# Performance work log

Measured on AMD Instinct MI355X. Metric: run time of the kernel, lower is better.

The kernel has to match this reference:

```python
import jax, jax.numpy as jnp
import numpy as np

B, T, NC, NK, H, W = 2, 4, 3, 16, 180, 320
K = 3
PAD = 1
SCALE = 4
K2 = K * K
CIN_D = T * NK  # deformable conv input channels = group_of_frames * num_kernels


def conv2d(x, w, b=None, pad=PAD):
    y = jax.lax.conv_general_dilated(
        x, w, (1, 1), [(pad, pad), (pad, pad)],
        dimension_numbers=('NCHW', 'OIHW', 'NCHW'))
    if b is not None:
        y = y + b[None, :, None, None]
    return y


def convlstm(X, w, b, W_ci, W_cf, W_co):
    # X: (B, T, NC, H, W) -> (B, T, NK, H, W); peephole ConvLSTM
    Bn = X.shape[0]
    h0 = jnp.zeros((Bn, NK, H, W), X.dtype)
    c0 = jnp.zeros_like(h0)

    def step(carry, xt):
        h, c = carry
        g = conv2d(jnp.concatenate([xt, h], axis=1), w, b)  # (B, 4*NK, H, W)
        ig, fg, cg, og = jnp.split(g, 4, axis=1)
        i = jax.nn.sigmoid(ig + W_ci * c)
        f = jax.nn.sigmoid(fg + W_cf * c)
        c = f * c + i * jnp.tanh(cg)
        o = jax.nn.sigmoid(og + W_co * c)
        h = o * jnp.tanh(c)
        return (h, c), h

    _, hs = jax.lax.scan(step, (h0, c0), jnp.swapaxes(X, 0, 1))
    return jnp.swapaxes(hs, 0, 1)  # (B, T, NK, H, W)


def deform_conv(x, off_w, off_b, mod_w, mod_b, w, b):
    # Modulated deformable conv v2 (torchvision deform_conv2d semantics)
    Bn, Cin, Hi, Wi = x.shape
    off = conv2d(x, off_w, off_b).reshape(Bn, K2, 2, Hi, Wi)  # (dy, dx) per tap
    mask = 2.0 * jax.nn.sigmoid(conv2d(x, mod_w, mod_b))       # (B, K2, H, W)
    dy, dx = off[:, :, 0], off[:, :, 1]
    ky, kx = jnp.meshgrid(jnp.arange(K), jnp.arange(K), indexing='ij')
    base_y = jnp.arange(Hi, dtype=x.dtype)[None, None, :, None] - PAD + ky.reshape(1, K2, 1, 1).astype(x.dtype)
    base_x = jnp.arange(Wi, dtype=x.dtype)[None, None, None, :] - PAD + kx.reshape(1, K2, 1, 1).astype(x.dtype)
    py = base_y + dy  # (B, K2, H, W) float sampling positions
    px = base_x + dx
    y0 = jnp.floor(py)
    x0 = jnp.floor(px)

    def gather(yi, xi):
        valid = ((yi >= 0) & (yi < Hi) & (xi >= 0) & (xi < Wi)).astype(x.dtype)
        yc = jnp.clip(yi, 0, Hi - 1).astype(jnp.int32)
        xc = jnp.clip(xi, 0, Wi - 1).astype(jnp.int32)
        v = jax.vmap(lambda xb, yb, xib: xb[:, yb, xib])(x, yc, xc)  # (B, C, K2, H, W)
        return v * valid[:, None]

    wy1 = py - y0
    wx1 = px - x0
    samp = (((1 - wy1) * (1 - wx1))[:, None] * gather(y0, x0)
            + ((1 - wy1) * wx1)[:, None] * gather(y0, x0 + 1)
            + (wy1 * (1 - wx1))[:, None] * gather(y0 + 1, x0)
            + (wy1 * wx1)[:, None] * gather(y0 + 1, x0 + 1))
    samp = samp * mask[:, None]  # (B, Cin, K2, H, W)
    out = jnp.einsum('bckhw,ock->bohw', samp, w.reshape(w.shape[0], Cin, K2))
    return out + b[None, :, None, None]


def pixel_shuffle(x, r):
    Bn, Crr, Hi, Wi = x.shape
    C = Crr // (r * r)
    x = x.reshape(Bn, C, r, r, Hi, Wi).transpose(0, 1, 4, 2, 5, 3)
    return x.reshape(Bn, C, Hi * r, Wi * r)


def setup_inputs() -> dict:
    key = jax.random.key(0)
    ks = jax.random.split(key, 16)
    s = lambda k, shape, sc=0.05: jax.random.normal(k, shape, jnp.float32) * sc
    return {
        'X': jax.random.uniform(ks[0], (B, T, NC, H, W), jnp.float32),
        'lstm_w': s(ks[1], (4 * NK, NC + NK, K, K)),
        'lstm_b': s(ks[2], (4 * NK,)),
        'W_ci': s(ks[3], (NK, H, W)),
        'W_cf': s(ks[4], (NK, H, W)),
        'W_co': s(ks[5], (NK, H, W)),
        'off_w': s(ks[6], (2 * K2, CIN_D, K, K), 0.01),
        'off_b': jnp.zeros((2 * K2,), jnp.float32),
        'mod_w': s(ks[7], (K2, CIN_D, K, K), 0.01),
        'mod_b': jnp.zeros((K2,), jnp.float32),
        'def_w': s(ks[8], (NK, CIN_D, K, K)),
        'def_b': s(ks[9], (NK,)),
        'out_w': s(ks[10], (NC * SCALE ** 2, NK, K, K)),
        'out_b': s(ks[11], (NC * SCALE ** 2,)),
    }


def reference(X, lstm_w, lstm_b, W_ci, W_cf, W_co, off_w, off_b, mod_w, mod_b, def_w, def_b, out_w, out_b):
    hs = convlstm(X, lstm_w, lstm_b, W_ci, W_cf, W_co)   # (B, T, NK, H, W)
    x = hs.reshape(hs.shape[0], T * NK, H, W)            # chunk(dim=1)+squeeze+cat(dim=1)
    x = deform_conv(x, off_w, off_b, mod_w, mod_b, def_w, def_b)  # (B, NK, H, W)
    x = conv2d(x, out_w, out_b)                          # (B, NC*scale^2, H, W)
    return jnp.clip(pixel_shuffle(x, SCALE), 0.0, 255.0)
```

## Files before the change

### kernel.cpp

```cpp
#include <hip/hip_runtime.h>
#include <hip/hip_bf16.h>

#define Bn 2
#define Tn 4
#define NCc 3
#define NKc 16
#define Hc 180
#define Wc 320
#define HWc (Hc * Wc)
#define NPIX (Bn * HWc)
#define CIN_LSTM 19
#define GATES 64
#define CIN_D 64
#define TAPS_L (CIN_LSTM * 9)
#define TAPS_D (CIN_D * 9)
#define TAPS_O (NKc * 9)

typedef __hip_bfloat16 bf16;
typedef float f32x4 __attribute__((ext_vector_type(4)));
typedef float f32x2 __attribute__((ext_vector_type(2)));

__device__ __forceinline__ float getv(const float* p, long i) { return p[i]; }
__device__ __forceinline__ float getv(const bf16* p, long i) {
    unsigned int u = ((unsigned int)((const unsigned short*)p)[i]) << 16;
    return __uint_as_float(u);
}
__device__ __forceinline__ void putv(float* p, long i, float v) { p[i] = v; }
__device__ __forceinline__ void putv(bf16* p, long i, float v) { p[i] = __float2bfloat16(v); }
__device__ __forceinline__ float sigm(float x) { return 1.0f / (1.0f + __expf(-x)); }
__device__ __forceinline__ float tanh_(float x) { return 1.0f - 2.0f / (__expf(2.0f * x) + 1.0f); }

__device__ __forceinline__ void load4(const float* row, int x0, float* d) {
    const float4 v = *(const float4*)(row + x0);
    d[0] = v.x; d[1] = v.y; d[2] = v.z; d[3] = v.w;
}
__device__ __forceinline__ void load4(const bf16* row, int x0, float* d) {
    ushort4 u = *(const ushort4*)((const unsigned short*)row + x0);
    d[0] = __uint_as_float(((unsigned int)u.x) << 16);
    d[1] = __uint_as_float(((unsigned int)u.y) << 16);
    d[2] = __uint_as_float(((unsigned int)u.z) << 16);
    d[3] = __uint_as_float(((unsigned int)u.w) << 16);
}

__device__ __forceinline__ int xcd_chunked(int i, int nwg) {
    int q = nwg >> 3, r = nwg & 7;
    int xcd = i & 7, idx = i >> 3;
    return (xcd < r ? xcd * (q + 1) : r * (q + 1) + (xcd - r) * q) + idx;
}

__device__ __forceinline__ void om_wait()
{
    asm volatile("s_waitcnt vmcnt(0)" ::: "memory");
    __builtin_amdgcn_sched_barrier(0);
}

__device__ __forceinline__ void om13_issue(
    const float* a0p, const float* a1p, const float* a2p,
    const float* b0p, const float* b1p, const float* b2p,
    const float* l0p, const float* l1p, const float* l2p,
    const float* r0p, const float* r1p, const float* r2p,
    f32x4& A0, f32x4& A1, f32x4& A2, f32x4& B0, f32x4& B1, f32x4& B2,
    float& l0, float& l1, float& l2, float& r0, float& r1, float& r2)
{
    asm volatile(
        "global_load_dwordx4 %[A0], %[a0], off\n\t"
        "global_load_dwordx4 %[A1], %[a1], off\n\t"
        "global_load_dwordx4 %[A2], %[a2], off\n\t"
        "global_load_dwordx4 %[B0], %[b0], off\n\t"
        "global_load_dwordx4 %[B1], %[b1], off\n\t"
        "global_load_dwordx4 %[B2], %[b2], off\n\t"
        "global_load_dword %[L0], %[l0p], off\n\t"
        "global_load_dword %[L1], %[l1p], off\n\t"
        "global_load_dword %[L2], %[l2p], off\n\t"
        "global_load_dword %[R0], %[r0p], off\n\t"
        "global_load_dword %[R1], %[r1p], off\n\t"
        "global_load_dword %[R2], %[r2p], off\n\t"
        : [A0]"=&v"(A0), [A1]"=&v"(A1), [A2]"=&v"(A2),
          [B0]"=&v"(B0), [B1]"=&v"(B1), [B2]"=&v"(B2),
          [L0]"=&v"(l0), [L1]"=&v"(l1), [L2]"=&v"(l2),
          [R0]"=&v"(r0), [R1]"=&v"(r1), [R2]"=&v"(r2)
        : [a0]"v"(a0p), [a1]"v"(a1p), [a2]"v"(a2p),
          [b0]"v"(b0p), [b1]"v"(b1p), [b2]"v"(b2p),
          [l0p]"v"(l0p), [l1p]"v"(l1p), [l2p]"v"(l2p),
          [r0p]"v"(r0p), [r1p]"v"(r1p), [r2p]"v"(r2p));
}

__device__ __forceinline__ void lstm_issue12(
    const float* p0, const float* p1, const float* p2, const float* p3,
    f32x4& a0, float& l0, float& r0,
    f32x4& a1, float& l1, float& r1,
    f32x4& a2, float& l2, float& r2,
    f32x4& a3, float& l3, float& r3)
{
    asm volatile(
        "global_load_dwordx4 %[A0], %[P0], off\n\t"
        "global_load_dword   %[L0], %[P0], off offset:-4\n\t"
        "global_load_dword   %[R0], %[P0], off offset:16\n\t"
        "global_load_dwordx4 %[A1], %[P1], off\n\t"
        "global_load_dword   %[L1], %[P1], off offset:-4\n\t"
        "global_load_dword   %[R1], %[P1], off offset:16\n\t"
        "global_load_dwordx4 %[A2], %[P2], off\n\t"
        "global_load_dword   %[L2], %[P2], off offset:-4\n\t"
        "global_load_dword   %[R2], %[P2], off offset:16\n\t"
        "global_load_dwordx4 %[A3], %[P3], off\n\t"
        "global_load_dword   %[L3], %[P3], off offset:-4\n\t"
        "global_load_dword   %[R3], %[P3], off offset:16\n\t"
        : [A0]"=&v"(a0), [L0]"=&v"(l0), [R0]"=&v"(r0),
          [A1]"=&v"(a1), [L1]"=&v"(l1), [R1]"=&v"(r1),
          [A2]"=&v"(a2), [L2]"=&v"(l2), [R2]"=&v"(r2),
          [A3]"=&v"(a3), [L3]"=&v"(l3), [R3]"=&v"(r3)
        : [P0]"v"(p0), [P1]"v"(p1), [P2]"v"(p2), [P3]"v"(p3));
}

__device__ __forceinline__ void dfm_issue9w(
    const float* base, const int (&o)[9], f32x2 (&v)[9])
{
    asm volatile(
        "global_load_dwordx2 %[V0], %[O0], %[B]\n\t"
        "global_load_dwordx2 %[V1], %[O1], %[B]\n\t"
        "global_load_dwordx2 %[V2], %[O2], %[B]\n\t"
        "global_load_dwordx2 %[V3], %[O3], %[B]\n\t"
        "global_load_dwordx2 %[V4], %[O4], %[B]\n\t"
        "global_load_dwordx2 %[V5], %[O5], %[B]\n\t"
        "global_load_dwordx2 %[V6], %[O6], %[B]\n\t"
        "global_load_dwordx2 %[V7], %[O7], %[B]\n\t"
        "global_load_dwordx2 %[V8], %[O8], %[B]\n\t"
        : [V0]"=&v"(v[0]), [V1]"=&v"(v[1]), [V2]"=&v"(v[2]),
          [V3]"=&v"(v[3]), [V4]"=&v"(v[4]), [V5]"=&v"(v[5]),
          [V6]"=&v"(v[6]), [V7]"=&v"(v[7]), [V8]"=&v"(v[8])
        : [B]"s"(base),
          [O0]"v"(o[0]), [O1]"v"(o[1]), [O2]"v"(o[2]),
          [O3]"v"(o[3]), [O4]"v"(o[4]), [O5]"v"(o[5]),
          [O6]"v"(o[6]), [O7]"v"(o[7]), [O8]"v"(o[8]));
}

__global__ void __launch_bounds__(256) k_detect(const void* lstm_w_raw, int* flag)
{
    __shared__ int bad;
    if (threadIdx.x == 0) bad = 0;
    __syncthreads();
    const unsigned short* u = (const unsigned short*)lstm_w_raw;
    int local = 0;
    for (int i = threadIdx.x; i < GATES * TAPS_L; i += 256) {
        unsigned int f32 = ((unsigned int)u[i]) << 16;
        float v = __uint_as_float(f32);
        if (!(fabsf(v) <= 64.0f)) local = 1;
    }
    if (local) atomicOr(&bad, 1);
    __syncthreads();
    if (threadIdx.x == 0) flag[0] = bad ? 0 : 1;
}

template <typename S>
__device__ __forceinline__ void conv_plane2r(
    const S* __restrict__ src, int cin, int y0, int x0, int kc,
    const float* __restrict__ sw, float (&acc)[2][4][4])
{
    float xs[4][6];
#pragma unroll
    for (int r = 0; r < 4; r++) {
        int yy = y0 - 1 + r;
        if (yy >= 0 && yy < Hc) {
            const S* row = src + (long)yy * Wc;
            xs[r][0] = (x0 > 0) ? getv(row, x0 - 1) : 0.0f;
            load4(row, x0, &xs[r][1]);
            xs[r][5] = (x0 + 4 < Wc) ? getv(row, x0 + 4) : 0.0f;
        } else {
#pragma unroll
            for (int j = 0; j < 6; j++) xs[r][j] = 0.0f;
        }
    }
    float4 wq[9];
#pragma unroll
    for (int t9 = 0; t9 < 9; t9++)
        wq[t9] = *(const float4*)&sw[(((cin * 9 + t9) * 16) + kc) * 4];
#pragma unroll
    for (int ky = 0; ky < 3; ky++) {
#pragma unroll
        for (int kx = 0; kx < 3; kx++) {
            const float4 w = wq[ky * 3 + kx];
#pragma unroll
            for (int px = 0; px < 4; px++) {
                float v0 = xs[ky][px + kx];
                float v1 = xs[ky + 1][px + kx];
                acc[0][0][px] += w.x * v0;  acc[1][0][px] += w.x * v1;
                acc[0][1][px] += w.y * v0;  acc[1][1][px] += w.y * v1;
                acc[0][2][px] += w.z * v0;  acc[1][2][px] += w.z * v1;
                acc[0][3][px] += w.w * v0;  acc[1][3][px] += w.w * v1;
            }
        }
    }
}

template <typename T>
__device__ __forceinline__ void lstm2r_body(
    const T* __restrict__ X, const T* __restrict__ lstm_w, const T* __restrict__ lstm_b,
    const T* __restrict__ Wci, const T* __restrict__ Wcf, const T* __restrict__ Wco,
    float* __restrict__ c_buf, float* __restrict__ xcat, int t,
    float* sw, float* sb)
{
    for (int i = threadIdx.x; i < GATES * TAPS_L; i += 256) {
        int co = i / TAPS_L, tap = i - co * TAPS_L;
        int kc = co & 15, g = co >> 4;
        sw[(tap * 16 + kc) * 4 + g] = getv(lstm_w, i);
    }
    if (threadIdx.x < GATES) sb[threadIdx.x] = getv(lstm_b, threadIdx.x);
    __syncthreads();

    int blk = xcd_chunked(blockIdx.x, Bn * 90 * 5);
    int seg = blk % 5; int rem = blk / 5;
    int yp = rem % 90; int b = rem / 90;
    int y0 = yp * 2;
    int kc = threadIdx.x >> 4, pl = threadIdx.x & 15;
    int x0 = seg * 64 + pl * 4;

    float acc[2][4][4];
#pragma unroll
    for (int px = 0; px < 4; px++) {
#pragma unroll
        for (int r = 0; r < 2; r++) {
            acc[r][0][px] = sb[kc];
            acc[r][1][px] = sb[16 + kc];
            acc[r][2][px] = sb[32 + kc];
            acc[r][3][px] = sb[48 + kc];
        }
    }

    const T* xt = X + (long)(b * Tn + t) * NCc * HWc;
#pragma unroll 1
    for (int cin = 0; cin < NCc; cin++)
        conv_plane2r(xt + (long)cin * HWc, cin, y0, x0, kc, sw, acc);

    if (t > 0) {
        const float* hp = xcat + ((long)b * CIN_D + (t - 1) * NKc) * HWc;
        long ro[4]; float vm[4];
#pragma unroll
        for (int r = 0; r < 4; r++) {
            int yy = y0 - 1 + r;
            vm[r] = (yy >= 0 && yy < Hc) ? 1.0f : 0.0f;
            ro[r] = (long)min(max(yy, 0), Hc - 1) * Wc + x0;
        }
        const float m0 = (x0 > 0) ? 1.0f : 0.0f;
        const float m1 = (x0 + 4 < Wc) ? 1.0f : 0.0f;

#pragma unroll 1
        for (int cin = 0; cin < NKc; cin++) {
            const float* xc = hp + (long)cin * HWc;
            f32x4 a0, a1, a2, a3;
            float l0, l1, l2, l3, rh0, rh1, rh2, rh3;
            lstm_issue12(xc + ro[0], xc + ro[1], xc + ro[2], xc + ro[3],
                         a0, l0, rh0, a1, l1, rh1, a2, l2, rh2, a3, l3, rh3);
            float4 wq[9];
#pragma unroll
            for (int t9 = 0; t9 < 9; t9++)
                wq[t9] = *(const float4*)&sw[((((cin + NCc) * 9 + t9) * 16) + kc) * 4];
            om_wait();
            float xs[4][6];
#pragma unroll
            for (int r = 0; r < 4; r++) {
                const f32x4 a = (r == 0) ? a0 : (r == 1) ? a1 : (r == 2) ? a2 : a3;
                const float ll = (r == 0) ? l0 : (r == 1) ? l1 : (r == 2) ? l2 : l3;
                const float rr = (r == 0) ? rh0 : (r == 1) ? rh1 : (r == 2) ? rh2 : rh3;
                xs[r][0] = ll * vm[r] * m0;
                xs[r][1] = a.x * vm[r]; xs[r][2] = a.y * vm[r];
                xs[r][3] = a.z * vm[r]; xs[r][4] = a.w * vm[r];
                xs[r][5] = rr * vm[r] * m1;
            }
#pragma unroll
            for (int ky = 0; ky < 3; ky++) {
#pragma unroll
                for (int kx = 0; kx < 3; kx++) {
                    const float4 w = wq[ky * 3 + kx];
#pragma unroll
                    for (int px = 0; px < 4; px++) {
                        float v0 = xs[ky][px + kx];
                        float v1 = xs[ky + 1][px + kx];
                        acc[0][0][px] += w.x * v0;  acc[1][0][px] += w.x * v1;
                        acc[0][1][px] += w.y * v0;  acc[1][1][px] += w.y * v1;
                        acc[0][2][px] += w.z * v0;  acc[1][2][px] += w.z * v1;
                        acc[0][3][px] += w.w * v0;  acc[1][3][px] += w.w * v1;
                    }
                }
            }
        }
    }

#pragma unroll
    for (int r = 0; r < 2; r++) {
        int y = y0 + r;
        long pbase = (long)y * Wc + x0;
        float* cb = c_buf + (long)(b * NKc + kc) * HWc + pbase;
        float cprev[4];
        if (t > 0) {
            const float4 cv = *(const float4*)cb;
            cprev[0] = cv.x; cprev[1] = cv.y; cprev[2] = cv.z; cprev[3] = cv.w;
        } else {
            cprev[0] = cprev[1] = cprev[2] = cprev[3] = 0.0f;
        }
        float wci[4], wcf[4], wco[4];
        load4(Wci + (long)kc * HWc + pbase, 0, wci);
        load4(Wcf + (long)kc * HWc + pbase, 0, wcf);
        load4(Wco + (long)kc * HWc + pbase, 0, wco);

        float cn4[4], h4[4];
#pragma unroll
        for (int px = 0; px < 4; px++) {
            float ii = sigm(acc[r][0][px] + wci[px] * cprev[px]);
            float ff = sigm(acc[r][1][px] + wcf[px] * cprev[px]);
            float cn = ff * cprev[px] + ii * tanh_(acc[r][2][px]);
            float oo = sigm(acc[r][3][px] + wco[px] * cn);
            cn4[px] = cn; h4[px] = oo * tanh_(cn);
        }
        *(float4*)cb = make_float4(cn4[0], cn4[1], cn4[2], cn4[3]);
        *(float4*)(xcat + ((long)b * CIN_D + t * NKc + kc) * HWc + pbase) =
            make_float4(h4[0], h4[1], h4[2], h4[3]);
    }
}

__global__ void __launch_bounds__(256) k_lstm2(
    const void* X, const void* lstm_w, const void* lstm_b,
    const void* Wci, const void* Wcf, const void* Wco,
    const int* __restrict__ flag,
    float* c_buf, float* xcat, int t)
{
    __shared__ float sw[TAPS_L * GATES];
    __shared__ float sb[GATES];
    if (flag[0])
        lstm2r_body<bf16>((const bf16*)X, (const bf16*)lstm_w, (const bf16*)lstm_b,
                          (const bf16*)Wci, (const bf16*)Wcf, (const bf16*)Wco,
                          c_buf, xcat, t, sw, sb);
    else
        lstm2r_body<float>((const float*)X, (const float*)lstm_w, (const float*)lstm_b,
                           (const float*)Wci, (const float*)Wcf, (const float*)Wco,
                           c_buf, xcat, t, sw, sb);
}

template <typename T>
__device__ __forceinline__ void offmod13_body(
    const float* __restrict__ xcat,
    const T* __restrict__ off_w, const T* __restrict__ off_b,
    const T* __restrict__ mod_w, const T* __restrict__ mod_b,
    float* __restrict__ offbuf, float* __restrict__ maskbuf,
    float* sw, float* sb)
{
    int rb = xcd_chunked(blockIdx.x, 450);
    int type = rb & 1;
    int chunk = rb >> 1;
    const int nslot = type ? 12 : 16;

    for (int i = threadIdx.x; i < TAPS_D * nslot; i += 256) {
        int tap = i / nslot, j = i - tap * nslot;
        int o = type ? 16 + j : j;
        float v = 0.0f;
        if (o < 18) v = getv(off_w, (long)o * TAPS_D + tap);
        else if (o < 27) v = getv(mod_w, (long)(o - 18) * TAPS_D + tap);
        sw[tap * nslot + j] = v;
    }
    if (threadIdx.x < nslot) {
        int o = (type ? 16 : 0) + threadIdx.x;
        sb[threadIdx.x] = (o < 18) ? getv(off_b, o)
                        : (o < 27 ? getv(mod_b, o - 18) : 0.0f);
    }
    __syncthreads();

    int og = threadIdx.x >> 6, lane = threadIdx.x & 63;

    long pg[2]; pg[0] = (long)chunk * 512 + 4 * lane; pg[1] = pg[0] + 256;
    int bg[2], ppg[2];
    int yo[2][3]; float vm[2][3], mL[2], mR[2];
    const float* xbg[2];
#pragma unroll
    for (int g = 0; g < 2; g++) {
        int b = (int)(pg[g] / HWc);
        int pp = (int)(pg[g] - (long)b * HWc);
        int y = pp / Wc, x = pp - (pp / Wc) * Wc;
        bg[g] = b; ppg[g] = pp;
        xbg[g] = xcat + (long)b * CIN_D * HWc;
#pragma unroll
        for (int ky = 0; ky < 3; ky++) {
            int yy = y + ky - 1;
            vm[g][ky] = (yy >= 0 && yy < Hc) ? 1.0f : 0.0f;
            yo[g][ky] = min(max(yy, 0), Hc - 1) * Wc + x;
        }
        mL[g] = (x > 0) ? 1.0f : 0.0f;
        mR[g] = (x + 4 < Wc) ? 1.0f : 0.0f;
    }
    const float *eLp[3], *eRp[3];
    {
        long pL = (long)chunk * 512;
        int b = (int)(pL / HWc); int pp = (int)(pL - (long)b * HWc);
        int y = pp / Wc, x = pp - (pp / Wc) * Wc;
#pragma unroll
        for (int ky = 0; ky < 3; ky++)
            eLp[ky] = xcat + (long)b * CIN_D * HWc
                    + (long)min(max(y + ky - 1, 0), Hc - 1) * Wc + x - 1;
        long pR = (long)chunk * 512 + 511;
        b = (int)(pR / HWc); pp = (int)(pR - (long)b * HWc);
        y = pp / Wc; x = pp - (pp / Wc) * Wc;
#pragma unroll
        for (int ky = 0; ky < 3; ky++)
            eRp[ky] = xcat + (long)b * CIN_D * HWc
                    + (long)min(max(y + ky - 1, 0), Hc - 1) * Wc + x + 1;
    }

    const int per = type ? 3 : 4;
    int jbase = og * per;
    const int upl = (lane + 63) & 63, dnl = (lane + 1) & 63;

    float acc[4][2][4];
#pragma unroll
    for (int j = 0; j < 4; j++) {
        float bv = (j < per) ? sb[jbase + j] : 0.0f;
#pragma unroll
        for (int g = 0; g < 2; g++)
#pragma unroll
            for (int px = 0; px < 4; px++) acc[j][g][px] = bv;
    }

#pragma unroll 1
    for (int cin = 0; cin < CIN_D; cin++) {
        const long coff = (long)cin * HWc;
        const float* c0 = xbg[0] + coff;
        const float* c1 = xbg[1] + coff;
        f32x4 A[3], B[3]; float el[3], er[3];
        om13_issue(c0 + yo[0][0], c0 + yo[0][1], c0 + yo[0][2],
                   c1 + yo[1][0], c1 + yo[1][1], c1 + yo[1][2],
                   eLp[0] + coff, eLp[1] + coff, eLp[2] + coff,
                   eRp[0] + coff, eRp[1] + coff, eRp[2] + coff,
                   A[0], A[1], A[2], B[0], B[1], B[2],
                   el[0], el[1], el[2], er[0], er[1], er[2]);
        float4 wr4[9]; float3 wr3[9];
        if (type == 0) {
#pragma unroll
            for (int t9 = 0; t9 < 9; t9++)
                wr4[t9] = *(const float4*)&sw[(cin * 9 + t9) * 16 + jbase];
        } else {
#pragma unroll
            for (int t9 = 0; t9 < 9; t9++) {
                const float* wp = &sw[(cin * 9 + t9) * 12 + jbase];
                wr3[t9] = make_float3(wp[0], wp[1], wp[2]);
            }
        }
        om_wait();

        float xs0[3][6], xs1[3][6];
#pragma unroll
        for (int ky = 0; ky < 3; ky++) {
            float aw = A[ky].w, ax = A[ky].x, bw = B[ky].w, bx = B[ky].x;
            float sAw = __shfl(aw, upl);
            float sAx = __shfl(ax, dnl);
            float sBw = __shfl(bw, upl);
            float sBx = __shfl(bx, dnl);
            float B0x = __shfl(bx, 0);
            float A63w = __shfl(aw, 63);
            float g0l = (lane == 0) ? el[ky] : sAw;
            float g0r = (lane == 63) ? B0x : sAx;
            float g1l = (lane == 0) ? A63w : sBw;
            float g1r = (lane == 63) ? er[ky] : sBx;
            float v0 = vm[0][ky], v1 = vm[1][ky];
            xs0[ky][0] = g0l * v0 * mL[0];
            xs0[ky][1] = A[ky].x * v0; xs0[ky][2] = A[ky].y * v0;
            xs0[ky][3] = A[ky].z * v0; xs0[ky][4] = A[ky].w * v0;
            xs0[ky][5] = g0r * v0 * mR[0];
            xs1[ky][0] = g1l * v1 * mL[1];
            xs1[ky][1] = B[ky].x * v1; xs1[ky][2] = B[ky].y * v1;
            xs1[ky][3] = B[ky].z * v1; xs1[ky][4] = B[ky].w * v1;
            xs1[ky][5] = g1r * v1 * mR[1];
        }

        if (type == 0) {
#pragma unroll
            for (int ky = 0; ky < 3; ky++) {
#pragma unroll
                for (int kx = 0; kx < 3; kx++) {
                    const float4 wq = wr4[ky * 3 + kx];
#pragma unroll
                    for (int px = 0; px < 4; px++) {
                        float u = xs0[ky][px + kx];
                        acc[0][0][px] += wq.x * u;
                        acc[1][0][px] += wq.y * u;
                        acc[2][0][px] += wq.z * u;
                        acc[3][0][px] += wq.w * u;
                        float w2 = xs1[ky][px + kx];
                        acc[0][1][px] += wq.x * w2;
                        acc[1][1][px] += wq.y * w2;
                        acc[2][1][px] += wq.z * w2;
                        acc[3][1][px] += wq.w * w2;
                    }
                }
            }
        } else {
#pragma unroll
            for (int ky = 0; ky < 3; ky++) {
#pragma unroll
                for (int kx = 0; kx < 3; kx++) {
                    const float3 wq = wr3[ky * 3 + kx];
#pragma unroll
                    for (int px = 0; px < 4; px++) {
                        float u = xs0[ky][px + kx];
                        acc[0][0][px] += wq.x * u;
                        acc[1][0][px] += wq.y * u;
                        acc[2][0][px] += wq.z * u;
                        float w2 = xs1[ky][px + kx];
                        acc[0][1][px] += wq.x * w2;
                        acc[1][1][px] += wq.y * w2;
                        acc[2][1][px] += wq.z * w2;
                    }
                }
            }
        }
    }

#pragma unroll
    for (int j = 0; j < 4; j++) {
        if (j >= per) break;
        int o = (type ? 16 : 0) + jbase + j;
        if (o >= 27) break;
        if (o < 18) {
#pragma unroll
            for (int g = 0; g < 2; g++) {
                float* dst = offbuf + ((long)bg[g] * 18 + o) * HWc + ppg[g];
                *(float4*)dst = make_float4(acc[j][g][0], acc[j][g][1],
                                            acc[j][g][2], acc[j][g][3]);
            }
        } else {
#pragma unroll
            for (int g = 0; g < 2; g++) {
                float* dst = maskbuf + ((long)bg[g] * 9 + (o - 18)) * HWc + ppg[g];
                *(float4*)dst = make_float4(
                    2.0f * sigm(acc[j][g][0]), 2.0f * sigm(acc[j][g][1]),
                    2.0f * sigm(acc[j][g][2]), 2.0f * sigm(acc[j][g][3]));
            }
        }
    }
}

__global__ void __launch_bounds__(256) k_offmod(
    const float* xcat, const void* off_w, const void* off_b,
    const void* mod_w, const void* mod_b, const int* __restrict__ flag,
    float* offbuf, float* maskbuf)
{
    __shared__ float sw[TAPS_D * 16];
    __shared__ float sb[16];
    if (flag[0])
        offmod13_body<bf16>(xcat, (const bf16*)off_w, (const bf16*)off_b,
                            (const bf16*)mod_w, (const bf16*)mod_b, offbuf, maskbuf, sw, sb);
    else
        offmod13_body<float>(xcat, (const float*)off_w, (const float*)off_b,
                             (const float*)mod_w, (const float*)mod_b, offbuf, maskbuf, sw, sb);
}

template <typename T>
__device__ __forceinline__ void deform5_body(
    const float* __restrict__ xcat, const float* __restrict__ offbuf,
    const float* __restrict__ maskbuf,
    const T* __restrict__ def_w, const T* __restrict__ def_b,
    float* __restrict__ dcout, float* sw, float* sb)
{
    for (int i = threadIdx.x; i < NKc * TAPS_D; i += 256) {
        int co = i / TAPS_D;
        int tap = i - co * TAPS_D;
        sw[tap * NKc + co] = getv(def_w, i);
    }
    if (threadIdx.x < NKc) sb[threadIdx.x] = getv(def_b, threadIdx.x);
    __syncthreads();

    int blk = xcd_chunked(blockIdx.x, NPIX / 256);
    int idx0 = blk * 256;
    int b = idx0 / HWc;
    int p = idx0 - b * HWc + threadIdx.x;
    int y = p / Wc, x = p - (p / Wc) * Wc;

    float w00[9], w01[9], w10[9], w11[9];
    int o0[9], o1[9];
    float sel[9];
#pragma unroll
    for (int k = 0; k < 9; k++) {
        int ky = k / 3, kx = k - (k / 3) * 3;
        float dy = offbuf[((long)b * 18 + 2 * k) * HWc + p];
        float dx = offbuf[((long)b * 18 + 2 * k + 1) * HWc + p];
        float m = maskbuf[((long)b * 9 + k) * HWc + p];
        float py = (float)(y - 1 + ky) + dy;
        float px = (float)(x - 1 + kx) + dx;
        float y0f = floorf(py), x0f = floorf(px);
        int y0 = (int)y0f, x0 = (int)x0f;
        float wy1 = py - y0f, wx1 = px - x0f;
        float a00 = (1.0f - wy1) * (1.0f - wx1) * m;
        float a01 = (1.0f - wy1) * wx1 * m;
        float a10 = wy1 * (1.0f - wx1) * m;
        float a11 = wy1 * wx1 * m;
        bool vy0 = (y0 >= 0) && (y0 < Hc);
        bool vy1 = (y0 + 1 >= 0) && (y0 + 1 < Hc);
        bool vx0 = (x0 >= 0) && (x0 < Wc);
        bool vx1 = (x0 + 1 >= 0) && (x0 + 1 < Wc);
        w00[k] = (vy0 && vx0) ? a00 : 0.0f;
        w01[k] = (vy0 && vx1) ? a01 : 0.0f;
        w10[k] = (vy1 && vx0) ? a10 : 0.0f;
        w11[k] = (vy1 && vx1) ? a11 : 0.0f;
        int yc0 = min(max(y0, 0), Hc - 1);
        int yc1 = min(max(y0 + 1, 0), Hc - 1);
        int xc0 = min(max(x0, 0), Wc - 1);
        int xc1 = min(max(x0 + 1, 0), Wc - 1);
        o0[k] = (yc0 * Wc + xc0) * 4;
        o1[k] = (yc1 * Wc + xc0) * 4;
        sel[k] = (xc1 > xc0) ? 1.0f : 0.0f;
    }

    float acc[NKc];
#pragma unroll
    for (int i = 0; i < NKc; i++) acc[i] = sb[i];

    const float* xb = xcat + (long)b * CIN_D * HWc;
#pragma unroll 1
    for (int cin = 0; cin < CIN_D; cin++) {
        const float* xc = xb + (long)cin * HWc;
        f32x2 u0[9], u1[9];
        dfm_issue9w(xc, o0, u0);
        dfm_issue9w(xc, o1, u1);
        om_wait();
        float s[9];
#pragma unroll
        for (int k = 0; k < 9; k++) {
            float v01 = u0[k].x + sel[k] * (u0[k].y - u0[k].x);
            float v11 = u1[k].x + sel[k] * (u1[k].y - u1[k].x);
            s[k] = w00[k] * u0[k].x + w01[k] * v01 +
                   w10[k] * u1[k].x + w11[k] * v11;
        }
#pragma unroll
        for (int k = 0; k < 9; k++) {
            const float* wrow = &sw[(cin * 9 + k) * NKc];
#pragma unroll
            for (int co = 0; co < NKc; co++) acc[co] += wrow[co] * s[k];
        }
    }

#pragma unroll
    for (int co = 0; co < NKc; co++)
        dcout[((long)b * NKc + co) * HWc + p] = acc[co];
}

__global__ void __launch_bounds__(256) k_deform(
    const float* xcat, const float* offbuf, const float* maskbuf,
    const void* def_w, const void* def_b, const int* __restrict__ flag,
    float* dcout)
{
    __shared__ float sw[TAPS_D * NKc];
    __shared__ float sb[NKc];
    if (flag[0])
        deform5_body<bf16>(xcat, offbuf, maskbuf, (const bf16*)def_w, (const bf16*)def_b,
                           dcout, sw, sb);
    else
        deform5_body<float>(xcat, offbuf, maskbuf, (const float*)def_w, (const float*)def_b,
                            dcout, sw, sb);
}

template <typename T>
__device__ __forceinline__ void outconv6_body(
    const float* __restrict__ dcout, const T* __restrict__ out_w,
    const T* __restrict__ out_b, T* __restrict__ out, float* sw, float* sb)
{
    int rb = xcd_chunked(blockIdx.x, 900);
    int type = rb & 1;
    int chunk = rb >> 1;

    for (int i = threadIdx.x; i < 24 * TAPS_O; i += 256) {
        int o = i / TAPS_O, tap = i - o * TAPS_O;
        int slot = (o / 6) * 8 + (o % 6);
        sw[tap * 32 + slot] = getv(out_w, (long)(type * 24 + o) * TAPS_O + tap);
    }
    if (threadIdx.x < 24) sb[threadIdx.x] = getv(out_b, type * 24 + threadIdx.x);
    __syncthreads();

    int og = threadIdx.x >> 6, lane = threadIdx.x & 63;
    long p0 = ((long)chunk * 64 + lane) * 4;
    int b = (int)(p0 / HWc);
    int p = (int)(p0 - (long)b * HWc);
    int y = p / Wc, x0 = p - (p / Wc) * Wc;

    float acc[6][4];
#pragma unroll
    for (int j = 0; j < 6; j++) {
        float bv = sb[og * 6 + j];
#pragma unroll
        for (int px = 0; px < 4; px++) acc[j][px] = bv;
    }

    const float* xb = dcout + (long)b * NKc * HWc;
#pragma unroll 1
    for (int cin = 0; cin < NKc; cin++) {
        const float* xc = xb + (long)cin * HWc;
        float xs[3][6];
#pragma unroll
        for (int ky = 0; ky < 3; ky++) {
            int yy = y + ky - 1;
            if (yy >= 0 && yy < Hc) {
                const float* row = xc + (long)yy * Wc;
                xs[ky][0] = (x0 > 0) ? row[x0 - 1] : 0.0f;
                load4(row, x0, &xs[ky][1]);
                xs[ky][5] = (x0 + 4 < Wc) ? row[x0 + 4] : 0.0f;
            } else {
#pragma unroll
                for (int j = 0; j < 6; j++) xs[ky][j] = 0.0f;
            }
        }
        float4 wa[9]; float2 wb[9];
#pragma unroll
        for (int t9 = 0; t9 < 9; t9++) {
            const float* wp = &sw[(cin * 9 + t9) * 32 + og * 8];
            wa[t9] = *(const float4*)wp;
            wb[t9] = *(const float2*)(wp + 4);
        }
#pragma unroll
        for (int ky = 0; ky < 3; ky++) {
#pragma unroll
            for (int kx = 0; kx < 3; kx++) {
                const float4 w0 = wa[ky * 3 + kx];
                const float2 w1 = wb[ky * 3 + kx];
#pragma unroll
                for (int px = 0; px < 4; px++) {
                    float v = xs[ky][px + kx];
                    acc[0][px] += w0.x * v;  acc[1][px] += w0.y * v;
                    acc[2][px] += w0.z * v;  acc[3][px] += w0.w * v;
                    acc[4][px] += w1.x * v;  acc[5][px] += w1.y * v;
                }
            }
        }
    }

#pragma unroll
    for (int j = 0; j < 6; j++) {
        int co = type * 24 + og * 6 + j;
        int cc = co >> 4;
        int r = co & 15;
        int ii = r >> 2, jj = r & 3;
        long ob = (((long)b * 3 + cc) * (Hc * 4) + (y * 4 + ii)) * (long)(Wc * 4);
#pragma unroll
        for (int px = 0; px < 4; px++) {
            float v = fminf(fmaxf(acc[j][px], 0.0f), 255.0f);
            putv(out, ob + (x0 + px) * 4 + jj, v);
        }
    }
}

__global__ void __launch_bounds__(256) k_outconv(
    const float* dcout, const void* out_w, const void* out_b,
    const int* __restrict__ flag, void* out)
{
    __shared__ float sw[TAPS_O * 32];
    __shared__ float sb[24];
    if (flag[0])
        outconv6_body<bf16>(dcout, (const bf16*)out_w, (const bf16*)out_b, (bf16*)out, sw, sb);
    else
        outconv6_body<float>(dcout, (const float*)out_w, (const float*)out_b, (float*)out, sw, sb);
}

extern "C" void kernel_launch(void* const* d_in, const int* in_sizes, int n_in,
                              void* d_out, int out_size, void* d_ws, size_t ws_size,
                              hipStream_t stream) {
    const void* X      = d_in[0];
    const void* lstm_w = d_in[1];
    const void* lstm_b = d_in[2];
    const void* Wci    = d_in[3];
    const void* Wcf    = d_in[4];
    const void* Wco    = d_in[5];
    const void* off_w  = d_in[6];
    const void* off_b  = d_in[7];
    const void* mod_w  = d_in[8];
    const void* mod_b  = d_in[9];
    const void* def_w  = d_in[10];
    const void* def_b  = d_in[11];
    const void* out_w  = d_in[12];
    const void* out_b  = d_in[13];

    int* flag = (int*)d_ws;
    float* W = (float*)d_ws + 64;
    size_t o = 0;
    float* c_buf   = W + o; o += (size_t)Bn * NKc * HWc;
    float* xcat    = W + o; o += (size_t)Bn * CIN_D * HWc;
    float* offbuf  = W + o; o += (size_t)Bn * 18 * HWc;
    float* maskbuf = W + o; o += (size_t)Bn * 9 * HWc;
    float* dcout   = W + o; o += (size_t)Bn * NKc * HWc;

    dim3 blk(256);
    dim3 gridP(NPIX / 256);
    dim3 gridL2(Bn * (Hc / 2) * 5);
    dim3 gridOM(2 * (NPIX / 512));
    dim3 gridC2(2 * (NPIX / 4 / 64));

    k_detect<<<1, blk, 0, stream>>>(lstm_w, flag);
    for (int t = 0; t < Tn; t++) {
        k_lstm2<<<gridL2, blk, 0, stream>>>(X, lstm_w, lstm_b, Wci, Wcf, Wco,
                                            flag, c_buf, xcat, t);
    }
    k_offmod<<<gridOM, blk, 0, stream>>>(xcat, off_w, off_b, mod_w, mod_b, flag,
                                         offbuf, maskbuf);
    k_deform<<<gridP, blk, 0, stream>>>(xcat, offbuf, maskbuf, def_w, def_b, flag, dcout);
    k_outconv<<<gridC2, blk, 0, stream>>>(dcout, out_w, out_b, flag, d_out);
}
```

Before: 575.6 us.

## Split offset/mask conv input channels across two block halves, sum in deform kernel

The offset/mask convolution now splits its 64 input channels into two halves handled by separate blocks. The grid doubles and each block's shared weight tile halves. Each half writes partial sums to its own offset and mask buffer, and the deform kernel adds the two partials and applies the mask sigmoid when it reads them. This trades extra partial-buffer writes and reads for more parallelism and lower shared-memory use per block, which should raise occupancy in the offset/mask stage.

```diff
diff --git a/kernel.cpp b/kernel.cpp
--- a/kernel.cpp
+++ b/kernel.cpp
@@ -336,30 +336,35 @@
 }
 
 template <typename T>
-__device__ __forceinline__ void offmod13_body(
+__device__ __forceinline__ void offmod16_body(
     const float* __restrict__ xcat,
     const T* __restrict__ off_w, const T* __restrict__ off_b,
     const T* __restrict__ mod_w, const T* __restrict__ mod_b,
-    float* __restrict__ offbuf, float* __restrict__ maskbuf,
+    float* __restrict__ ob0, float* __restrict__ mb0,
+    float* __restrict__ ob1, float* __restrict__ mb1,
     float* sw, float* sb)
 {
-    int rb = xcd_chunked(blockIdx.x, 450);
+    int rb = xcd_chunked(blockIdx.x, 900);
     int type = rb & 1;
-    int chunk = rb >> 1;
+    int half = (rb >> 1) & 1;
+    int chunk = rb >> 2;
     const int nslot = type ? 12 : 16;
 
-    for (int i = threadIdx.x; i < TAPS_D * nslot; i += 256) {
-        int tap = i / nslot, j = i - tap * nslot;
+    for (int i = threadIdx.x; i < 288 * nslot; i += 256) {
+        int tl = i / nslot, j = i - tl * nslot;
         int o = type ? 16 + j : j;
+        long gtap = (long)half * 288 + tl;
         float v = 0.0f;
-        if (o < 18) v = getv(off_w, (long)o * TAPS_D + tap);
-        else if (o < 27) v = getv(mod_w, (long)(o - 18) * TAPS_D + tap);
-        sw[tap * nslot + j] = v;
+        if (o < 18) v = getv(off_w, (long)o * TAPS_D + gtap);
+        else if (o < 27) v = getv(mod_w, (long)(o - 18) * TAPS_D + gtap);
+        sw[tl * nslot + j] = v;
     }
     if (threadIdx.x < nslot) {
         int o = (type ? 16 : 0) + threadIdx.x;
-        sb[threadIdx.x] = (o < 18) ? getv(off_b, o)
-                        : (o < 27 ? getv(mod_b, o - 18) : 0.0f);
+        float bv = 0.0f;
+        if (half == 0)
+            bv = (o < 18) ? getv(off_b, o) : (o < 27 ? getv(mod_b, o - 18) : 0.0f);
+        sb[threadIdx.x] = bv;
     }
     __syncthreads();
 
@@ -392,14 +397,14 @@
         int y = pp / Wc, x = pp - (pp / Wc) * Wc;
 #pragma unroll
         for (int ky = 0; ky < 3; ky++)
-            eLp[ky] = xcat + (long)b * CIN_D * HWc
+            eLp[ky] = xcat + ((long)b * CIN_D + half * 32) * HWc
                     + (long)min(max(y + ky - 1, 0), Hc - 1) * Wc + x - 1;
         long pR = (long)chunk * 512 + 511;
         b = (int)(pR / HWc); pp = (int)(pR - (long)b * HWc);
         y = pp / Wc; x = pp - (pp / Wc) * Wc;
 #pragma unroll
         for (int ky = 0; ky < 3; ky++)
-            eRp[ky] = xcat + (long)b * CIN_D * HWc
+            eRp[ky] = xcat + ((long)b * CIN_D + half * 32) * HWc
                     + (long)min(max(y + ky - 1, 0), Hc - 1) * Wc + x + 1;
     }
 
@@ -417,27 +422,29 @@
             for (int px = 0; px < 4; px++) acc[j][g][px] = bv;
     }
 
+    const long cbase = (long)half * 32 * HWc;
 #pragma unroll 1
-    for (int cin = 0; cin < CIN_D; cin++) {
-        const long coff = (long)cin * HWc;
+    for (int lc = 0; lc < 32; lc++) {
+        const long coff = cbase + (long)lc * HWc;
+        const long eoff = (long)lc * HWc;
         const float* c0 = xbg[0] + coff;
         const float* c1 = xbg[1] + coff;
         f32x4 A[3], B[3]; float el[3], er[3];
         om13_issue(c0 + yo[0][0], c0 + yo[0][1], c0 + yo[0][2],
                    c1 + yo[1][0], c1 + yo[1][1], c1 + yo[1][2],
-                   eLp[0] + coff, eLp[1] + coff, eLp[2] + coff,
-                   eRp[0] + coff, eRp[1] + coff, eRp[2] + coff,
+                   eLp[0] + eoff, eLp[1] + eoff, eLp[2] + eoff,
+                   eRp[0] + eoff, eRp[1] + eoff, eRp[2] + eoff,
                    A[0], A[1], A[2], B[0], B[1], B[2],
                    el[0], el[1], el[2], er[0], er[1], er[2]);
         float4 wr4[9]; float3 wr3[9];
         if (type == 0) {
 #pragma unroll
             for (int t9 = 0; t9 < 9; t9++)
-                wr4[t9] = *(const float4*)&sw[(cin * 9 + t9) * 16 + jbase];
+                wr4[t9] = *(const float4*)&sw[(lc * 9 + t9) * 16 + jbase];
         } else {
 #pragma unroll
             for (int t9 = 0; t9 < 9; t9++) {
-                const float* wp = &sw[(cin * 9 + t9) * 12 + jbase];
+                const float* wp = &sw[(lc * 9 + t9) * 12 + jbase];
                 wr3[t9] = make_float3(wp[0], wp[1], wp[2]);
             }
         }
@@ -511,6 +518,8 @@
         }
     }
 
+    float* obuf = half ? ob1 : ob0;
+    float* mbuf = half ? mb1 : mb0;
 #pragma unroll
     for (int j = 0; j < 4; j++) {
         if (j >= per) break;
@@ -519,17 +528,16 @@
         if (o < 18) {
 #pragma unroll
             for (int g = 0; g < 2; g++) {
-                float* dst = offbuf + ((long)bg[g] * 18 + o) * HWc + ppg[g];
+                float* dst = obuf + ((long)bg[g] * 18 + o) * HWc + ppg[g];
                 *(float4*)dst = make_float4(acc[j][g][0], acc[j][g][1],
                                             acc[j][g][2], acc[j][g][3]);
             }
         } else {
 #pragma unroll
             for (int g = 0; g < 2; g++) {
-                float* dst = maskbuf + ((long)bg[g] * 9 + (o - 18)) * HWc + ppg[g];
-                *(float4*)dst = make_float4(
-                    2.0f * sigm(acc[j][g][0]), 2.0f * sigm(acc[j][g][1]),
-                    2.0f * sigm(acc[j][g][2]), 2.0f * sigm(acc[j][g][3]));
+                float* dst = mbuf + ((long)bg[g] * 9 + (o - 18)) * HWc + ppg[g];
+                *(float4*)dst = make_float4(acc[j][g][0], acc[j][g][1],
+                                            acc[j][g][2], acc[j][g][3]);
             }
         }
     }
@@ -538,22 +546,25 @@
 __global__ void __launch_bounds__(256) k_offmod(
     const float* xcat, const void* off_w, const void* off_b,
     const void* mod_w, const void* mod_b, const int* __restrict__ flag,
-    float* offbuf, float* maskbuf)
-{
-    __shared__ float sw[TAPS_D * 16];
+    float* ob0, float* mb0, float* ob1, float* mb1)
+{
+    __shared__ float sw[288 * 16];
     __shared__ float sb[16];
     if (flag[0])
-        offmod13_body<bf16>(xcat, (const bf16*)off_w, (const bf16*)off_b,
-                            (const bf16*)mod_w, (const bf16*)mod_b, offbuf, maskbuf, sw, sb);
+        offmod16_body<bf16>(xcat, (const bf16*)off_w, (const bf16*)off_b,
+                            (const bf16*)mod_w, (const bf16*)mod_b,
+                            ob0, mb0, ob1, mb1, sw, sb);
     else
-        offmod13_body<float>(xcat, (const float*)off_w, (const float*)off_b,
-                             (const float*)mod_w, (const float*)mod_b, offbuf, maskbuf, sw, sb);
+        offmod16_body<float>(xcat, (const float*)off_w, (const float*)off_b,
+                             (const float*)mod_w, (const float*)mod_b,
+                             ob0, mb0, ob1, mb1, sw, sb);
 }
 
 template <typename T>
-__device__ __forceinline__ void deform5_body(
-    const float* __restrict__ xcat, const float* __restrict__ offbuf,
-    const float* __restrict__ maskbuf,
+__device__ __forceinline__ void deform6_body(
+    const float* __restrict__ xcat,
+    const float* __restrict__ ob0, const float* __restrict__ mb0,
+    const float* __restrict__ ob1, const float* __restrict__ mb1,
     const T* __restrict__ def_w, const T* __restrict__ def_b,
     float* __restrict__ dcout, float* sw, float* sb)
 {
@@ -577,9 +588,12 @@
 #pragma unroll
     for (int k = 0; k < 9; k++) {
         int ky = k / 3, kx = k - (k / 3) * 3;
-        float dy = offbuf[((long)b * 18 + 2 * k) * HWc + p];
-        float dx = offbuf[((long)b * 18 + 2 * k + 1) * HWc + p];
-        float m = maskbuf[((long)b * 9 + k) * HWc + p];
+        long oyi = ((long)b * 18 + 2 * k) * HWc + p;
+        long oxi = ((long)b * 18 + 2 * k + 1) * HWc + p;
+        long mi  = ((long)b * 9 + k) * HWc + p;
+        float dy = ob0[oyi] + ob1[oyi];
+        float dx = ob0[oxi] + ob1[oxi];
+        float m = 2.0f * sigm(mb0[mi] + mb1[mi]);
         float py = (float)(y - 1 + ky) + dy;
         float px = (float)(x - 1 + kx) + dx;
         float y0f = floorf(py), x0f = floorf(px);
@@ -640,18 +654,19 @@
 }
 
 __global__ void __launch_bounds__(256) k_deform(
-    const float* xcat, const float* offbuf, const float* maskbuf,
+    const float* xcat, const float* ob0, const float* mb0,
+    const float* ob1, const float* mb1,
     const void* def_w, const void* def_b, const int* __restrict__ flag,
     float* dcout)
 {
     __shared__ float sw[TAPS_D * NKc];
     __shared__ float sb[NKc];
     if (flag[0])
-        deform5_body<bf16>(xcat, offbuf, maskbuf, (const bf16*)def_w, (const bf16*)def_b,
-                           dcout, sw, sb);
+        deform6_body<bf16>(xcat, ob0, mb0, ob1, mb1,
+                           (const bf16*)def_w, (const bf16*)def_b, dcout, sw, sb);
     else
-        deform5_body<float>(xcat, offbuf, maskbuf, (const float*)def_w, (const float*)def_b,
-                            dcout, sw, sb);
+        deform6_body<float>(xcat, ob0, mb0, ob1, mb1,
+                            (const float*)def_w, (const float*)def_b, dcout, sw, sb);
 }
 
 template <typename T>
@@ -777,14 +792,16 @@
     size_t o = 0;
     float* c_buf   = W + o; o += (size_t)Bn * NKc * HWc;
     float* xcat    = W + o; o += (size_t)Bn * CIN_D * HWc;
+    float* dcout   = W + o; o += (size_t)Bn * NKc * HWc;
     float* offbuf  = W + o; o += (size_t)Bn * 18 * HWc;
     float* maskbuf = W + o; o += (size_t)Bn * 9 * HWc;
-    float* dcout   = W + o; o += (size_t)Bn * NKc * HWc;
+    float* offbuf1  = W + o; o += (size_t)Bn * 18 * HWc;
+    float* maskbuf1 = W + o; o += (size_t)Bn * 9 * HWc;
 
     dim3 blk(256);
     dim3 gridP(NPIX / 256);
     dim3 gridL2(Bn * (Hc / 2) * 5);
-    dim3 gridOM(2 * (NPIX / 512));
+    dim3 gridOM(4 * (NPIX / 512));
     dim3 gridC2(2 * (NPIX / 4 / 64));
 
     k_detect<<<1, blk, 0, stream>>>(lstm_w, flag);
@@ -793,7 +810,8 @@
                                             flag, c_buf, xcat, t);
     }
     k_offmod<<<gridOM, blk, 0, stream>>>(xcat, off_w, off_b, mod_w, mod_b, flag,
-                                         offbuf, maskbuf);
-    k_deform<<<gridP, blk, 0, stream>>>(xcat, offbuf, maskbuf, def_w, def_b, flag, dcout);
+                                         offbuf, maskbuf, offbuf1, maskbuf1);
+    k_deform<<<gridP, blk, 0, stream>>>(xcat, offbuf, maskbuf, offbuf1, maskbuf1,
+                                        def_w, def_b, flag, dcout);
     k_outconv<<<gridC2, blk, 0, stream>>>(dcout, out_w, out_b, flag, d_out);
 }
```

Measured after the change: 576.7 us. Within noise of the previous version (+0.2%).
